# Kernel tuning notes

Measured on AMD Instinct MI355X. Metric: run time of the kernel, lower is better.

Reference implementation:

```python
import jax, jax.numpy as jnp
import numpy as np
from jax import lax

B, Ht, Wt, C, NH, KV, FF = 32, 32, 32, 768, 12, 16, 4
HD = C // NH
EPS = 1e-5


def setup_inputs() -> dict:
    key = jax.random.key(0)
    ks = jax.random.split(key, 12)
    rn = lambda k, s, sc=0.02: jax.random.normal(k, s, jnp.float32) * sc
    inp = {"x": jax.random.normal(ks[0], (B, Ht * Wt, C), jnp.float32)}
    inp["ln1_g"] = jnp.ones((C,), jnp.float32)
    inp["ln1_b"] = jnp.zeros((C,), jnp.float32)
    for i, nm in enumerate(["q", "k", "v"]):
        inp[f"dw_w_{nm}"] = rn(ks[1 + i], (C, 1, 3, 3), 0.1)
        inp[f"dw_b_{nm}"] = jnp.zeros((C,), jnp.float32)
        inp[f"bn_g_{nm}"] = jnp.ones((C,), jnp.float32)
        inp[f"bn_b_{nm}"] = jnp.zeros((C,), jnp.float32)
        inp[f"bn_m_{nm}"] = jnp.zeros((C,), jnp.float32)
        inp[f"bn_v_{nm}"] = jnp.ones((C,), jnp.float32)
        inp[f"W_{nm}"] = rn(ks[4 + i], (C, C))
        inp[f"b_{nm}"] = jnp.zeros((C,), jnp.float32)
    inp["ln2_g"] = jnp.ones((C,), jnp.float32)
    inp["ln2_b"] = jnp.zeros((C,), jnp.float32)
    inp["W1"] = rn(ks[7], (FF * C, C))
    inp["b1"] = jnp.zeros((FF * C,), jnp.float32)
    inp["W2"] = rn(ks[8], (C, FF * C))
    inp["b2"] = jnp.zeros((C,), jnp.float32)
    return inp


def _ln(x, g, b):
    m = jnp.mean(x, -1, keepdims=True)
    v = jnp.var(x, -1, keepdims=True)
    return (x - m) * lax.rsqrt(v + EPS) * g + b


def _dw_branch(x4, w, bias, g, bb, m, v, stride):
    # depthwise conv (groups=C) -> ELU -> BatchNorm (eval) -> b (h w) c
    y = lax.conv_general_dilated(
        x4, w, (stride, stride), [(1, 1), (1, 1)],
        feature_group_count=C,
        dimension_numbers=("NCHW", "OIHW", "NCHW"),
    ) + bias[None, :, None, None]
    y = jax.nn.elu(y)
    y = (y - m[None, :, None, None]) * lax.rsqrt(v + EPS)[None, :, None, None] \
        * g[None, :, None, None] + bb[None, :, None, None]
    return y.reshape(B, C, -1).transpose(0, 2, 1)  # (B, n, C)


def _heads(t, Wm, bm):
    t = t @ Wm.T + bm                         # (B, n, C)
    n = t.shape[1]
    return t.reshape(B, n, NH, HD).transpose(0, 2, 1, 3)  # (B, H, n, d)


def reference(x, ln1_g, ln1_b,
              dw_w_q, dw_b_q, bn_g_q, bn_b_q, bn_m_q, bn_v_q, W_q, b_q,
              dw_w_k, dw_b_k, bn_g_k, bn_b_k, bn_m_k, bn_v_k, W_k, b_k,
              dw_w_v, dw_b_v, bn_g_v, bn_b_v, bn_m_v, bn_v_v, W_v, b_v,
              ln2_g, ln2_b, W1, b1, W2, b2):
    xn = _ln(x, ln1_g, ln1_b)
    x4 = xn.transpose(0, 2, 1).reshape(B, C, Ht, Wt)
    q = _heads(_dw_branch(x4, dw_w_q, dw_b_q, bn_g_q, bn_b_q, bn_m_q, bn_v_q, 1), W_q, b_q)
    k = _heads(_dw_branch(x4, dw_w_k, dw_b_k, bn_g_k, bn_b_k, bn_m_k, bn_v_k, 2), W_k, b_k)
    v = _heads(_dw_branch(x4, dw_w_v, dw_b_v, bn_g_v, bn_b_v, bn_m_v, bn_v_v, 2), W_v, b_v)
    scale = 1.0 / (HD ** 0.5)
    attn = jnp.einsum("bhnd,bhmd->bhnm", q, k) * scale
    attn = jax.nn.softmax(attn, axis=-1)
    o = jnp.einsum("bhnm,bhmd->bhnd", attn, v)
    o = o.transpose(0, 2, 1, 3).reshape(B, Ht * Wt, C)
    x = x + o  # DropPath is identity at inference
    h = _ln(x, ln2_g, ln2_b)
    h = jax.nn.gelu(h @ W1.T + b1, approximate=False) @ W2.T + b2
    return x + h
```

## Files before the change

kernel.cpp:

```cpp
#include <hip/hip_runtime.h>
#include <math.h>

#define NB   32
#define C_   768
#define NQ   1024
#define NKV  256
#define NH_  12
#define HD_  64
#define FFC  3072
#define EPS_ 1e-5f

typedef __attribute__((ext_vector_type(8))) _Float16 f16x8;
typedef __attribute__((ext_vector_type(4))) _Float16 f16x4;
typedef __attribute__((ext_vector_type(4))) float    f32x4;

__device__ __forceinline__ void gload_lds16(const void* g, void* l) {
  __builtin_amdgcn_global_load_lds((const __attribute__((address_space(1))) void*)g,
                                   (__attribute__((address_space(3))) void*)l, 16, 0, 0);
}

__global__ __launch_bounds__(256)
void ln_fwd_kernel(const float* __restrict__ x, const float* __restrict__ g,
                   const float* __restrict__ b, float* __restrict__ out) {
  const int row = blockIdx.x;
  const float* xr = x + (size_t)row * C_;
  const int t = threadIdx.x;
  float v0 = xr[t], v1 = xr[t + 256], v2 = xr[t + 512];
  float s = v0 + v1 + v2;
  float q = v0 * v0 + v1 * v1 + v2 * v2;
#pragma unroll
  for (int m = 1; m < 64; m <<= 1) { s += __shfl_xor(s, m); q += __shfl_xor(q, m); }
  __shared__ float ls[4], lq[4];
  const int w = t >> 6, lane = t & 63;
  if (lane == 0) { ls[w] = s; lq[w] = q; }
  __syncthreads();
  s = ls[0] + ls[1] + ls[2] + ls[3];
  q = lq[0] + lq[1] + lq[2] + lq[3];
  const float mean = s * (1.f / C_);
  const float rstd = rsqrtf(q * (1.f / C_) - mean * mean + EPS_);
  float* orow = out + (size_t)row * C_;
  orow[t]       = (v0 - mean) * rstd * g[t]       + b[t];
  orow[t + 256] = (v1 - mean) * rstd * g[t + 256] + b[t + 256];
  orow[t + 512] = (v2 - mean) * rstd * g[t + 512] + b[t + 512];
}

__global__ __launch_bounds__(256)
void resln2_kernel(const float* __restrict__ x, const float* __restrict__ o,
                   const float* __restrict__ g, const float* __restrict__ bb,
                   float* __restrict__ xr_out, _Float16* __restrict__ h) {
  const int row = blockIdx.x;
  const float* xp = x + (size_t)row * C_;
  const float* op = o + (size_t)row * C_;
  const int t = threadIdx.x;
  float v[3]; float s = 0.f, q = 0.f;
#pragma unroll
  for (int i = 0; i < 3; i++) {
    int c = t + i * 256;
    v[i] = xp[c] + op[c];
    s += v[i]; q += v[i] * v[i];
  }
#pragma unroll
  for (int m = 1; m < 64; m <<= 1) { s += __shfl_xor(s, m); q += __shfl_xor(q, m); }
  __shared__ float ls[4], lq[4];
  const int w = t >> 6, lane = t & 63;
  if (lane == 0) { ls[w] = s; lq[w] = q; }
  __syncthreads();
  s = ls[0] + ls[1] + ls[2] + ls[3];
  q = lq[0] + lq[1] + lq[2] + lq[3];
  const float mean = s * (1.f / C_);
  const float rstd = rsqrtf(q * (1.f / C_) - mean * mean + EPS_);
#pragma unroll
  for (int i = 0; i < 3; i++) {
    int c = t + i * 256;
    xr_out[(size_t)row * C_ + c] = v[i];
    h[(size_t)row * C_ + c] = (_Float16)((v[i] - mean) * rstd * g[c] + bb[c]);
  }
}

__global__ void cast_f16_kernel(const float* __restrict__ in, _Float16* __restrict__ out, int n) {
  int i = blockIdx.x * 256 + threadIdx.x;
  int stride = gridDim.x * 256;
  for (; i < n; i += stride) out[i] = (_Float16)in[i];
}

__global__ __launch_bounds__(256)
void vtrans_kernel(const _Float16* __restrict__ vbuf, _Float16* __restrict__ vT) {
  const int b = blockIdx.z;
  const int c = blockIdx.y * 256 + threadIdx.x;
  const int kvb = blockIdx.x * 64;
#pragma unroll
  for (int kk = 0; kk < 8; kk++) {
    int kv0 = kvb + kk * 8;
    f16x8 v;
#pragma unroll
    for (int j = 0; j < 8; j++)
      v[j] = vbuf[(size_t)((b << 8) + kv0 + j) * C_ + c];
    *(f16x8*)(vT + ((size_t)(b * C_ + c) << 8) + kv0) = v;
  }
}

struct DwP { const float *w, *bias, *g, *b, *m, *v; };

__global__ __launch_bounds__(256)
void dw_fused_kernel(const float* __restrict__ xn, DwP pq, DwP pk, DwP pv,
                     _Float16* __restrict__ oq, _Float16* __restrict__ ok,
                     _Float16* __restrict__ ov) {
  const int pos = blockIdx.x;
  const int b = pos >> 8;
  const int i = (pos >> 4) & 15, j = pos & 15;
  const float* xb = xn + (size_t)b * NQ * C_;
  for (int c = threadIdx.x; c < C_; c += 256) {
    float t[5][5];
#pragma unroll
    for (int u = 0; u < 5; u++) {
      int ih = 2 * i - 1 + u;
#pragma unroll
      for (int vv = 0; vv < 5; vv++) {
        int iw = 2 * j - 1 + vv;
        t[u][vv] = (ih >= 0 && ih < 32 && iw >= 0 && iw < 32)
                       ? xb[(size_t)(ih * 32 + iw) * C_ + c] : 0.f;
      }
    }
    float wq[9], wk[9], wv[9];
#pragma unroll
    for (int u = 0; u < 9; u++) {
      wq[u] = pq.w[c * 9 + u]; wk[u] = pk.w[c * 9 + u]; wv[u] = pv.w[c * 9 + u];
    }
    float ak = pk.bias[c], av = pv.bias[c];
#pragma unroll
    for (int u = 0; u < 3; u++)
#pragma unroll
      for (int vv = 0; vv < 3; vv++) {
        ak += t[u][vv] * wk[u * 3 + vv];
        av += t[u][vv] * wv[u * 3 + vv];
      }
    ak = ak > 0.f ? ak : expf(ak) - 1.f;
    av = av > 0.f ? av : expf(av) - 1.f;
    ak = (ak - pk.m[c]) * rsqrtf(pk.v[c] + EPS_) * pk.g[c] + pk.b[c];
    av = (av - pv.m[c]) * rsqrtf(pv.v[c] + EPS_) * pv.g[c] + pv.b[c];
    ok[((size_t)b * NKV + i * 16 + j) * C_ + c] = (_Float16)ak;
    ov[((size_t)b * NKV + i * 16 + j) * C_ + c] = (_Float16)av;
    float sq = rsqrtf(pq.v[c] + EPS_) * pq.g[c];
#pragma unroll
    for (int a = 0; a < 2; a++)
#pragma unroll
      for (int b2 = 0; b2 < 2; b2++) {
        float aq = pq.bias[c];
#pragma unroll
        for (int u = 0; u < 3; u++)
#pragma unroll
          for (int vv = 0; vv < 3; vv++)
            aq += t[a + u][b2 + vv] * wq[u * 3 + vv];
        aq = aq > 0.f ? aq : expf(aq) - 1.f;
        aq = (aq - pq.m[c]) * sq + pq.b[c];
        oq[((size_t)b * NQ + (2 * i + a) * 32 + (2 * j + b2)) * C_ + c] = (_Float16)aq;
      }
  }
}

__device__ __forceinline__ void stage_tile(const _Float16* __restrict__ src, int ldk,
                                           int row0, int kt, _Float16* lds, int w, int lane) {
#pragma unroll
  for (int it = 0; it < 4; it++) {
    int cid = (it * 4 + w) * 64 + lane;
    int row = cid >> 3, kg = cid & 7;
    int kgs = kg ^ (row & 7);
    const _Float16* g = src + (size_t)(row0 + row) * ldk + kt * 64 + kgs * 8;
    gload_lds16((const void*)g, (void*)((char*)lds + (it * 4 + w) * 1024));
  }
}

template <int EPI>
__global__ __launch_bounds__(256, 2)
void gemm_f16(const _Float16* __restrict__ A, const _Float16* __restrict__ Bw,
              const float* __restrict__ bias,
              _Float16* __restrict__ outh, float* __restrict__ outf,
              int M, int N, int K) {
  __shared__ __align__(16) _Float16 lds[2][2][128 * 64];
  const int tid = threadIdx.x, w = tid >> 6, lane = tid & 63;
  const int wm = w >> 1, wn = w & 1;
  const int m0 = blockIdx.x * 128, n0 = blockIdx.y * 128;

  f32x4 acc[4][4];
#pragma unroll
  for (int i = 0; i < 4; i++)
#pragma unroll
    for (int j = 0; j < 4; j++)
#pragma unroll
      for (int r = 0; r < 4; r++) acc[i][j][r] = 0.f;

  stage_tile(A, K, m0, 0, lds[0][0], w, lane);
  stage_tile(Bw, K, n0, 0, lds[0][1], w, lane);
  __syncthreads();
  const int NKT = K >> 6;
  int buf = 0;
  for (int kt = 0; kt < NKT; kt++) {
    if (kt + 1 < NKT) {
      stage_tile(A, K, m0, kt + 1, lds[buf ^ 1][0], w, lane);
      stage_tile(Bw, K, n0, kt + 1, lds[buf ^ 1][1], w, lane);
    }
    f16x8 af[4][2], bfr[4][2];
#pragma unroll
    for (int mi = 0; mi < 4; mi++)
#pragma unroll
      for (int kh = 0; kh < 2; kh++) {
        int row = wm * 64 + mi * 16 + (lane & 15);
        int kg = kh * 4 + (lane >> 4);
        af[mi][kh] = *(const f16x8*)&lds[buf][0][row * 64 + ((kg ^ (row & 7)) << 3)];
      }
#pragma unroll
    for (int ni = 0; ni < 4; ni++)
#pragma unroll
      for (int kh = 0; kh < 2; kh++) {
        int row = wn * 64 + ni * 16 + (lane & 15);
        int kg = kh * 4 + (lane >> 4);
        bfr[ni][kh] = *(const f16x8*)&lds[buf][1][row * 64 + ((kg ^ (row & 7)) << 3)];
      }
#pragma unroll
    for (int mi = 0; mi < 4; mi++)
#pragma unroll
      for (int ni = 0; ni < 4; ni++)
#pragma unroll
        for (int kh = 0; kh < 2; kh++)
          acc[mi][ni] = __builtin_amdgcn_mfma_f32_16x16x32_f16(af[mi][kh], bfr[ni][kh],
                                                               acc[mi][ni], 0, 0, 0);
    __syncthreads();
    buf ^= 1;
  }
#pragma unroll
  for (int mi = 0; mi < 4; mi++)
#pragma unroll
    for (int ni = 0; ni < 4; ni++) {
      int col = n0 + wn * 64 + ni * 16 + (lane & 15);
      float bv = bias[col];
#pragma unroll
      for (int r = 0; r < 4; r++) {
        int rowg = m0 + wm * 64 + mi * 16 + (lane >> 4) * 4 + r;
        float val = acc[mi][ni][r] + bv;
        size_t idx = (size_t)rowg * N + col;
        if (EPI == 0) {
          outh[idx] = (_Float16)val;
        } else if (EPI == 1) {
          float ge = 0.5f * val * (1.f + erff(val * 0.70710678118f));
          outh[idx] = (_Float16)ge;
        } else {
          outf[idx] += val;
        }
      }
    }
}

__global__ __launch_bounds__(512, 2)
void attn_kernel(const _Float16* __restrict__ Q, const _Float16* __restrict__ Kb,
                 const _Float16* __restrict__ vT, float* __restrict__ O) {
  __shared__ __align__(16) _Float16 Klds[256 * 64];
  __shared__ __align__(16) _Float16 Vt[64 * 256];
  const int tid = threadIdx.x, w = tid >> 6, lane = tid & 63;
  const int hi = lane >> 4, lo = lane & 15;
  const int half = blockIdx.x & 1;
  const int h = (blockIdx.x >> 1) % NH_;
  const int b = blockIdx.x / (2 * NH_);

  const _Float16* qp = Q + (size_t)b * NQ * C_ + h * HD_;
  const _Float16* kp = Kb + (size_t)b * NKV * C_ + h * HD_;
  const _Float16* vp = vT + ((size_t)(b * C_ + h * HD_) << 8);

#pragma unroll
  for (int i = 0; i < 4; i++) {
    int cid = i * 512 + w * 64 + lane;
    int row = cid >> 3, kg = cid & 7;
    const _Float16* g = kp + (size_t)row * C_ + ((kg ^ (row & 7)) << 3);
    gload_lds16((const void*)g, (void*)((char*)Klds + (i * 512 + w * 64) * 16));
  }
#pragma unroll
  for (int i = 0; i < 4; i++) {
    int cid = i * 512 + w * 64 + lane;
    int row = cid >> 5, kg = cid & 31;
    const _Float16* g = vp + ((size_t)row << 8) + ((kg ^ (row & 7)) << 3);
    gload_lds16((const void*)g, (void*)((char*)Vt + (i * 512 + w * 64) * 16));
  }
  __syncthreads();

#pragma unroll
  for (int ti = 0; ti < 4; ti++) {
    const int q0 = half * 512 + w * 64 + ti * 16;
    f16x8 qf[2];
#pragma unroll
    for (int kh = 0; kh < 2; kh++)
      qf[kh] = *(const f16x8*)(qp + (size_t)(q0 + lo) * C_ + kh * 32 + hi * 8);
    f32x4 S[16];
#pragma unroll
    for (int nt = 0; nt < 16; nt++) {
      f32x4 s; s[0] = 0.f; s[1] = 0.f; s[2] = 0.f; s[3] = 0.f;
      const _Float16* krow = &Klds[(nt * 16 + lo) * 64];
#pragma unroll
      for (int kh = 0; kh < 2; kh++) {
        f16x8 kf = *(const f16x8*)&krow[((kh * 4 + hi) ^ (lo & 7)) << 3];
        s = __builtin_amdgcn_mfma_f32_16x16x32_f16(kf, qf[kh], s, 0, 0, 0);
      }
      S[nt] = s;
    }
    float mx = -1e30f;
#pragma unroll
    for (int nt = 0; nt < 16; nt++)
#pragma unroll
      for (int r = 0; r < 4; r++) { S[nt][r] *= 0.125f; mx = fmaxf(mx, S[nt][r]); }
    mx = fmaxf(mx, __shfl_xor(mx, 16));
    mx = fmaxf(mx, __shfl_xor(mx, 32));
    float sum = 0.f;
#pragma unroll
    for (int nt = 0; nt < 16; nt++)
#pragma unroll
      for (int r = 0; r < 4; r++) { float e = __expf(S[nt][r] - mx); S[nt][r] = e; sum += e; }
    sum += __shfl_xor(sum, 16);
    sum += __shfl_xor(sum, 32);
    const float inv = 1.f / sum;
    f16x8 pa8[8];
#pragma unroll
    for (int ntp = 0; ntp < 8; ntp++)
#pragma unroll
      for (int r = 0; r < 4; r++) {
        pa8[ntp][r]     = (_Float16)(S[2 * ntp][r] * inv);
        pa8[ntp][4 + r] = (_Float16)(S[2 * ntp + 1][r] * inv);
      }
    f32x4 acc[4];
#pragma unroll
    for (int dt = 0; dt < 4; dt++) { acc[dt][0] = 0.f; acc[dt][1] = 0.f; acc[dt][2] = 0.f; acc[dt][3] = 0.f; }
#pragma unroll
    for (int dt = 0; dt < 4; dt++) {
      const int d = dt * 16 + lo, sw = d & 7;
      const _Float16* vrow = &Vt[d * 256 + 4 * (hi & 1)];
#pragma unroll
      for (int ntp = 0; ntp < 8; ntp++) {
        f16x4 v0 = *(const f16x4*)&vrow[((4 * ntp + (hi >> 1)) ^ sw) << 3];
        f16x4 v1 = *(const f16x4*)&vrow[((4 * ntp + 2 + (hi >> 1)) ^ sw) << 3];
        f16x8 vt8;
#pragma unroll
        for (int r = 0; r < 4; r++) { vt8[r] = v0[r]; vt8[4 + r] = v1[r]; }
        acc[dt] = __builtin_amdgcn_mfma_f32_16x16x32_f16(pa8[ntp], vt8, acc[dt], 0, 0, 0);
      }
    }
#pragma unroll
    for (int dt = 0; dt < 4; dt++)
#pragma unroll
      for (int r = 0; r < 4; r++)
        O[(size_t)(b * NQ + q0 + 4 * hi + r) * C_ + h * HD_ + dt * 16 + lo] = acc[dt][r];
  }
}

extern "C" void kernel_launch(void* const* d_in, const int* in_sizes, int n_in,
                              void* d_out, int out_size, void* d_ws, size_t ws_size,
                              hipStream_t stream) {
  (void)in_sizes; (void)n_in; (void)out_size; (void)ws_size;
  const float* x    = (const float*)d_in[0];
  const float* ln1g = (const float*)d_in[1];
  const float* ln1b = (const float*)d_in[2];
  DwP pq { (const float*)d_in[3], (const float*)d_in[4], (const float*)d_in[5],
           (const float*)d_in[6], (const float*)d_in[7], (const float*)d_in[8] };
  const float* Wq = (const float*)d_in[9];  const float* bq = (const float*)d_in[10];
  DwP pk { (const float*)d_in[11], (const float*)d_in[12], (const float*)d_in[13],
           (const float*)d_in[14], (const float*)d_in[15], (const float*)d_in[16] };
  const float* Wk = (const float*)d_in[17]; const float* bk = (const float*)d_in[18];
  DwP pv { (const float*)d_in[19], (const float*)d_in[20], (const float*)d_in[21],
           (const float*)d_in[22], (const float*)d_in[23], (const float*)d_in[24] };
  const float* Wv = (const float*)d_in[25]; const float* bv = (const float*)d_in[26];
  const float* ln2g = (const float*)d_in[27];
  const float* ln2b = (const float*)d_in[28];
  const float* W1 = (const float*)d_in[29]; const float* b1 = (const float*)d_in[30];
  const float* W2 = (const float*)d_in[31]; const float* b2 = (const float*)d_in[32];

  char* ws = (char*)d_ws;
  float*    xn   = (float*)(ws + 0);
  float*    o    = xn;
  _Float16* tq   = (_Float16*)(ws + 100663296);
  _Float16* tk   = (_Float16*)(ws + 150994944);
  _Float16* tv   = (_Float16*)(ws + 163577856);
  _Float16* hb   = tq;
  _Float16* vTb  = tv;
  _Float16* qb   = (_Float16*)(ws + 176160768);
  _Float16* gbuf = qb;
  _Float16* kb   = (_Float16*)(ws + 226492416);
  _Float16* vbuf = (_Float16*)(ws + 239075328);
  _Float16* wqh  = (_Float16*)(ws + 251658240);
  _Float16* wkh  = (_Float16*)(ws + 252837888);
  _Float16* wvh  = (_Float16*)(ws + 254017536);
  _Float16* w1h  = (_Float16*)(ws + 255197184);
  _Float16* w2h  = (_Float16*)(ws + 259915776);
  float* out = (float*)d_out;

  ln_fwd_kernel<<<NB * NQ, 256, 0, stream>>>(x, ln1g, ln1b, xn);
  cast_f16_kernel<<<1024, 256, 0, stream>>>(Wq, wqh, C_ * C_);
  cast_f16_kernel<<<1024, 256, 0, stream>>>(Wk, wkh, C_ * C_);
  cast_f16_kernel<<<1024, 256, 0, stream>>>(Wv, wvh, C_ * C_);
  cast_f16_kernel<<<2048, 256, 0, stream>>>(W1, w1h, FFC * C_);
  cast_f16_kernel<<<2048, 256, 0, stream>>>(W2, w2h, C_ * FFC);
  dw_fused_kernel<<<NB * 256, 256, 0, stream>>>(xn, pq, pk, pv, tq, tk, tv);
  gemm_f16<0><<<dim3(256, 6), 256, 0, stream>>>(tq, wqh, bq, qb, nullptr, NB * NQ, C_, C_);
  gemm_f16<0><<<dim3(64, 6), 256, 0, stream>>>(tk, wkh, bk, kb, nullptr, NB * NKV, C_, C_);
  gemm_f16<0><<<dim3(64, 6), 256, 0, stream>>>(tv, wvh, bv, vbuf, nullptr, NB * NKV, C_, C_);
  vtrans_kernel<<<dim3(4, 3, NB), 256, 0, stream>>>(vbuf, vTb);
  attn_kernel<<<NB * NH_ * 2, 512, 0, stream>>>(qb, kb, vTb, o);
  resln2_kernel<<<NB * NQ, 256, 0, stream>>>(x, o, ln2g, ln2b, out, hb);
  for (int mc = 0; mc < 4; mc++) {
    gemm_f16<1><<<dim3(64, 24), 256, 0, stream>>>(hb + (size_t)mc * 8192 * C_, w1h, b1,
                                                  gbuf, nullptr, 8192, FFC, C_);
    gemm_f16<2><<<dim3(64, 6), 256, 0, stream>>>(gbuf, w2h, b2, nullptr,
                                                 out + (size_t)mc * 8192 * C_, 8192, C_, FFC);
  }
}
```

Baseline: 960.1 us.

## Store LN1 and attention outputs in fp16, merge weight casts, restructure depthwise conv

The LN1 output and the attention output are now written as fp16 instead of fp32, halving that intermediate traffic. The five weight-cast launches are merged into one kernel. The depthwise conv kernel now gives each thread one channel and one output row, and reuses a sliding 5x5 window across 16 columns. It also hoists weight and BN constant loads and folds BN into a single scale and shift. The cost is lower intermediate precision and a smaller grid for the conv kernel.

New measurement: 930.6 us. 3.1% less time.

```diff
diff --git a/kernel.cpp b/kernel.cpp
--- a/kernel.cpp
+++ b/kernel.cpp
@@ -21,7 +21,7 @@
 
 __global__ __launch_bounds__(256)
 void ln_fwd_kernel(const float* __restrict__ x, const float* __restrict__ g,
-                   const float* __restrict__ b, float* __restrict__ out) {
+                   const float* __restrict__ b, _Float16* __restrict__ out) {
   const int row = blockIdx.x;
   const float* xr = x + (size_t)row * C_;
   const int t = threadIdx.x;
@@ -38,25 +38,25 @@
   q = lq[0] + lq[1] + lq[2] + lq[3];
   const float mean = s * (1.f / C_);
   const float rstd = rsqrtf(q * (1.f / C_) - mean * mean + EPS_);
-  float* orow = out + (size_t)row * C_;
-  orow[t]       = (v0 - mean) * rstd * g[t]       + b[t];
-  orow[t + 256] = (v1 - mean) * rstd * g[t + 256] + b[t + 256];
-  orow[t + 512] = (v2 - mean) * rstd * g[t + 512] + b[t + 512];
+  _Float16* orow = out + (size_t)row * C_;
+  orow[t]       = (_Float16)((v0 - mean) * rstd * g[t]       + b[t]);
+  orow[t + 256] = (_Float16)((v1 - mean) * rstd * g[t + 256] + b[t + 256]);
+  orow[t + 512] = (_Float16)((v2 - mean) * rstd * g[t + 512] + b[t + 512]);
 }
 
 __global__ __launch_bounds__(256)
-void resln2_kernel(const float* __restrict__ x, const float* __restrict__ o,
+void resln2_kernel(const float* __restrict__ x, const _Float16* __restrict__ o,
                    const float* __restrict__ g, const float* __restrict__ bb,
                    float* __restrict__ xr_out, _Float16* __restrict__ h) {
   const int row = blockIdx.x;
   const float* xp = x + (size_t)row * C_;
-  const float* op = o + (size_t)row * C_;
+  const _Float16* op = o + (size_t)row * C_;
   const int t = threadIdx.x;
   float v[3]; float s = 0.f, q = 0.f;
 #pragma unroll
   for (int i = 0; i < 3; i++) {
     int c = t + i * 256;
-    v[i] = xp[c] + op[c];
+    v[i] = xp[c] + (float)op[c];
     s += v[i]; q += v[i] * v[i];
   }
 #pragma unroll
@@ -77,10 +77,24 @@
   }
 }
 
-__global__ void cast_f16_kernel(const float* __restrict__ in, _Float16* __restrict__ out, int n) {
+#define SZ_CC (C_ * C_)
+#define SZ_CF (FFC * C_)
+__global__ void cast_all_kernel(const float* __restrict__ Wq, const float* __restrict__ Wk,
+                                const float* __restrict__ Wv, const float* __restrict__ W1,
+                                const float* __restrict__ W2,
+                                _Float16* __restrict__ oq, _Float16* __restrict__ ok,
+                                _Float16* __restrict__ ov, _Float16* __restrict__ o1,
+                                _Float16* __restrict__ o2) {
+  const int total = 3 * SZ_CC + 2 * SZ_CF;
   int i = blockIdx.x * 256 + threadIdx.x;
   int stride = gridDim.x * 256;
-  for (; i < n; i += stride) out[i] = (_Float16)in[i];
+  for (; i < total; i += stride) {
+    if (i < SZ_CC)                     oq[i] = (_Float16)Wq[i];
+    else if (i < 2 * SZ_CC)            ok[i - SZ_CC] = (_Float16)Wk[i - SZ_CC];
+    else if (i < 3 * SZ_CC)            ov[i - 2 * SZ_CC] = (_Float16)Wv[i - 2 * SZ_CC];
+    else if (i < 3 * SZ_CC + SZ_CF)    o1[i - 3 * SZ_CC] = (_Float16)W1[i - 3 * SZ_CC];
+    else                               o2[i - 3 * SZ_CC - SZ_CF] = (_Float16)W2[i - 3 * SZ_CC - SZ_CF];
+  }
 }
 
 __global__ __launch_bounds__(256)
@@ -101,32 +115,49 @@
 
 struct DwP { const float *w, *bias, *g, *b, *m, *v; };
 
+__device__ __forceinline__ float elu_f(float x) {
+  return x > 0.f ? x : __expf(x) - 1.f;
+}
+
 __global__ __launch_bounds__(256)
-void dw_fused_kernel(const float* __restrict__ xn, DwP pq, DwP pk, DwP pv,
+void dw_fused_kernel(const _Float16* __restrict__ xn, DwP pq, DwP pk, DwP pv,
                      _Float16* __restrict__ oq, _Float16* __restrict__ ok,
                      _Float16* __restrict__ ov) {
-  const int pos = blockIdx.x;
-  const int b = pos >> 8;
-  const int i = (pos >> 4) & 15, j = pos & 15;
-  const float* xb = xn + (size_t)b * NQ * C_;
-  for (int c = threadIdx.x; c < C_; c += 256) {
-    float t[5][5];
+  const int i = blockIdx.x;
+  const int b = blockIdx.z;
+  const int c = blockIdx.y * 256 + threadIdx.x;
+  const _Float16* xb = xn + (size_t)b * NQ * C_ + c;
+
+  float wq[9], wk[9], wv[9];
+#pragma unroll
+  for (int u = 0; u < 9; u++) {
+    wq[u] = pq.w[c * 9 + u]; wk[u] = pk.w[c * 9 + u]; wv[u] = pv.w[c * 9 + u];
+  }
+  const float skq = rsqrtf(pq.v[c] + EPS_) * pq.g[c], bnq = pq.b[c] - pq.m[c] * skq;
+  const float skk = rsqrtf(pk.v[c] + EPS_) * pk.g[c], bnk = pk.b[c] - pk.m[c] * skk;
+  const float skv = rsqrtf(pv.v[c] + EPS_) * pv.g[c], bnv = pv.b[c] - pv.m[c] * skv;
+  const float cbq = pq.bias[c], cbk = pk.bias[c], cbv = pv.bias[c];
+
+  float t[5][5];
+  auto ldc = [&](int s, int iw) {
+    const bool cv = (iw >= 0 && iw < 32);
 #pragma unroll
     for (int u = 0; u < 5; u++) {
       int ih = 2 * i - 1 + u;
-#pragma unroll
-      for (int vv = 0; vv < 5; vv++) {
-        int iw = 2 * j - 1 + vv;
-        t[u][vv] = (ih >= 0 && ih < 32 && iw >= 0 && iw < 32)
-                       ? xb[(size_t)(ih * 32 + iw) * C_ + c] : 0.f;
-      }
-    }
-    float wq[9], wk[9], wv[9];
-#pragma unroll
-    for (int u = 0; u < 9; u++) {
-      wq[u] = pq.w[c * 9 + u]; wk[u] = pk.w[c * 9 + u]; wv[u] = pv.w[c * 9 + u];
-    }
-    float ak = pk.bias[c], av = pv.bias[c];
+      t[u][s] = (cv && ih >= 0 && ih < 32) ? (float)xb[(size_t)(ih * 32 + iw) * C_] : 0.f;
+    }
+  };
+
+#pragma unroll
+  for (int j = 0; j < 16; j++) {
+    if (j == 0) {
+      ldc(0, -1); ldc(1, 0); ldc(2, 1); ldc(3, 2); ldc(4, 3);
+    } else {
+#pragma unroll
+      for (int u = 0; u < 5; u++) { t[u][0] = t[u][2]; t[u][1] = t[u][3]; t[u][2] = t[u][4]; }
+      ldc(3, 2 * j + 2); ldc(4, 2 * j + 3);
+    }
+    float ak = cbk, av = cbv;
 #pragma unroll
     for (int u = 0; u < 3; u++)
 #pragma unroll
@@ -134,25 +165,21 @@
         ak += t[u][vv] * wk[u * 3 + vv];
         av += t[u][vv] * wv[u * 3 + vv];
       }
-    ak = ak > 0.f ? ak : expf(ak) - 1.f;
-    av = av > 0.f ? av : expf(av) - 1.f;
-    ak = (ak - pk.m[c]) * rsqrtf(pk.v[c] + EPS_) * pk.g[c] + pk.b[c];
-    av = (av - pv.m[c]) * rsqrtf(pv.v[c] + EPS_) * pv.g[c] + pv.b[c];
+    ak = elu_f(ak) * skk + bnk;
+    av = elu_f(av) * skv + bnv;
     ok[((size_t)b * NKV + i * 16 + j) * C_ + c] = (_Float16)ak;
     ov[((size_t)b * NKV + i * 16 + j) * C_ + c] = (_Float16)av;
-    float sq = rsqrtf(pq.v[c] + EPS_) * pq.g[c];
 #pragma unroll
     for (int a = 0; a < 2; a++)
 #pragma unroll
       for (int b2 = 0; b2 < 2; b2++) {
-        float aq = pq.bias[c];
+        float aq = cbq;
 #pragma unroll
         for (int u = 0; u < 3; u++)
 #pragma unroll
           for (int vv = 0; vv < 3; vv++)
             aq += t[a + u][b2 + vv] * wq[u * 3 + vv];
-        aq = aq > 0.f ? aq : expf(aq) - 1.f;
-        aq = (aq - pq.m[c]) * sq + pq.b[c];
+        aq = elu_f(aq) * skq + bnq;
         oq[((size_t)b * NQ + (2 * i + a) * 32 + (2 * j + b2)) * C_ + c] = (_Float16)aq;
       }
   }
@@ -252,7 +279,7 @@
 
 __global__ __launch_bounds__(512, 2)
 void attn_kernel(const _Float16* __restrict__ Q, const _Float16* __restrict__ Kb,
-                 const _Float16* __restrict__ vT, float* __restrict__ O) {
+                 const _Float16* __restrict__ vT, _Float16* __restrict__ O) {
   __shared__ __align__(16) _Float16 Klds[256 * 64];
   __shared__ __align__(16) _Float16 Vt[64 * 256];
   const int tid = threadIdx.x, w = tid >> 6, lane = tid & 63;
@@ -344,7 +371,7 @@
     for (int dt = 0; dt < 4; dt++)
 #pragma unroll
       for (int r = 0; r < 4; r++)
-        O[(size_t)(b * NQ + q0 + 4 * hi + r) * C_ + h * HD_ + dt * 16 + lo] = acc[dt][r];
+        O[(size_t)(b * NQ + q0 + 4 * hi + r) * C_ + h * HD_ + dt * 16 + lo] = (_Float16)acc[dt][r];
   }
 }
 
@@ -370,8 +397,8 @@
   const float* W2 = (const float*)d_in[31]; const float* b2 = (const float*)d_in[32];
 
   char* ws = (char*)d_ws;
-  float*    xn   = (float*)(ws + 0);
-  float*    o    = xn;
+  _Float16* xn   = (_Float16*)(ws + 0);
+  _Float16* o    = xn;
   _Float16* tq   = (_Float16*)(ws + 100663296);
   _Float16* tk   = (_Float16*)(ws + 150994944);
   _Float16* tv   = (_Float16*)(ws + 163577856);
@@ -389,12 +416,8 @@
   float* out = (float*)d_out;
 
   ln_fwd_kernel<<<NB * NQ, 256, 0, stream>>>(x, ln1g, ln1b, xn);
-  cast_f16_kernel<<<1024, 256, 0, stream>>>(Wq, wqh, C_ * C_);
-  cast_f16_kernel<<<1024, 256, 0, stream>>>(Wk, wkh, C_ * C_);
-  cast_f16_kernel<<<1024, 256, 0, stream>>>(Wv, wvh, C_ * C_);
-  cast_f16_kernel<<<2048, 256, 0, stream>>>(W1, w1h, FFC * C_);
-  cast_f16_kernel<<<2048, 256, 0, stream>>>(W2, w2h, C_ * FFC);
-  dw_fused_kernel<<<NB * 256, 256, 0, stream>>>(xn, pq, pk, pv, tq, tk, tv);
+  cast_all_kernel<<<2048, 256, 0, stream>>>(Wq, Wk, Wv, W1, W2, wqh, wkh, wvh, w1h, w2h);
+  dw_fused_kernel<<<dim3(16, 3, NB), 256, 0, stream>>>(xn, pq, pk, pv, tq, tk, tv);
   gemm_f16<0><<<dim3(256, 6), 256, 0, stream>>>(tq, wqh, bq, qb, nullptr, NB * NQ, C_, C_);
   gemm_f16<0><<<dim3(64, 6), 256, 0, stream>>>(tk, wkh, bk, kb, nullptr, NB * NKV, C_, C_);
   gemm_f16<0><<<dim3(64, 6), 256, 0, stream>>>(tv, wvh, bv, vbuf, nullptr, NB * NKV, C_, C_);
```
